# Kernel optimization log

Hardware: AMD Instinct MI355X
Metric: run time of the kernel (lower is better)

Reference implementation:

```python
import jax, jax.numpy as jnp
import numpy as np

EPS = 1e-5

def _ln(x, g, b):
    mu = x.mean(-1, keepdims=True)
    var = ((x - mu) ** 2).mean(-1, keepdims=True)
    return (x - mu) / jnp.sqrt(var + EPS) * g + b

def setup_inputs() -> dict:
    key = jax.random.key(0)
    ks = jax.random.split(key, 24)
    B, S, I, H, D, F = 64, 512, 32, 64, 128, 256
    def w(k, shape, fan_in):
        return jax.random.uniform(k, shape, jnp.float32, -1.0, 1.0) / np.sqrt(fan_in)
    return {
        'x': jax.random.normal(ks[0], (B, S, I), jnp.float32),
        'W_ih': w(ks[1], (H, I), H), 'b_ih': w(ks[2], (H,), H),
        'W_hh': w(ks[3], (H, H), H), 'b_hh': w(ks[4], (H,), H),
        'Wp': w(ks[5], (D, H), H), 'bp': w(ks[6], (D,), H),
        'Wqkv': w(ks[7], (3 * D, D), D), 'bqkv': jnp.zeros((3 * D,), jnp.float32),
        'Wo': w(ks[8], (D, D), D), 'bo': jnp.zeros((D,), jnp.float32),
        'g1': jnp.ones((D,), jnp.float32), 'be1': jnp.zeros((D,), jnp.float32),
        'W1': w(ks[9], (F, D), D), 'b1': w(ks[10], (F,), D),
        'W2': w(ks[11], (D, F), F), 'b2': w(ks[12], (D,), F),
        'g2': jnp.ones((D,), jnp.float32), 'be2': jnp.zeros((D,), jnp.float32),
        'gn': jnp.ones((D,), jnp.float32), 'bn': jnp.zeros((D,), jnp.float32),
        'Wf': w(ks[13], (I, D), D), 'bf': w(ks[14], (I,), D),
    }

def reference(x, W_ih, b_ih, W_hh, b_hh, Wp, bp, Wqkv, bqkv, Wo, bo,
              g1, be1, W1, b1, W2, b2, g2, be2, gn, bn, Wf, bf):
    B, S, I = x.shape
    H = W_ih.shape[0]
    D = Wp.shape[0]
    nh = 8
    hd = D // nh

    # RNNCell tanh recurrence over time (sequential, vectorized over batch)
    xs = jnp.swapaxes(x, 0, 1)  # (S, B, I)
    def step(h, x_t):
        h = jnp.tanh(x_t @ W_ih.T + b_ih + h @ W_hh.T + b_hh)
        return h, h
    _, hs = jax.lax.scan(step, jnp.zeros((B, H), x.dtype), xs)  # (S, B, H)

    proj = hs @ Wp.T + bp  # (S, B, D)

    # TransformerEncoderLayer (post-norm, relu), dropout = identity (eval)
    qkv = proj @ Wqkv.T + bqkv  # (S, B, 3D)
    q, k, v = jnp.split(qkv, 3, axis=-1)
    q = q.reshape(S, B, nh, hd)
    k = k.reshape(S, B, nh, hd)
    v = v.reshape(S, B, nh, hd)
    scores = jnp.einsum('sbhd,tbhd->bhst', q, k) / np.sqrt(hd)
    attn = jax.nn.softmax(scores, axis=-1)
    ctx = jnp.einsum('bhst,tbhd->sbhd', attn, v).reshape(S, B, D)
    attn_out = ctx @ Wo.T + bo
    x1 = _ln(proj + attn_out, g1, be1)
    ff = jax.nn.relu(x1 @ W1.T + b1) @ W2.T + b2
    x2 = _ln(x1 + ff, g2, be2)

    out = _ln(x2 + proj, gn, bn)
    pooled = out.mean(axis=0)  # (B, D)
    return jnp.tanh(pooled @ Wf.T + bf)
```

## Files before the change

### kernel.cpp

```cpp
#include <hip/hip_runtime.h>
#include <hip/hip_bf16.h>

#define BB 64
#define SS 512
#define II 32
#define HH 64
#define DD 128
#define FF 256
#define NHEAD 8
#define HDIM 16
#define NTOK (SS*BB)

typedef short bf16x8 __attribute__((ext_vector_type(8)));
typedef float f32x4  __attribute__((ext_vector_type(4)));

__device__ __forceinline__ float fast_tanh(float x) {
    float ax = fabsf(x);
    float e = __expf(-2.0f * ax);
    float r = (1.0f - e) * __builtin_amdgcn_rcpf(1.0f + e);
    return copysignf(r, x);
}

__device__ __forceinline__ float bcast(float v, int lane) {
    return __int_as_float(__builtin_amdgcn_readlane(__float_as_int(v), lane));
}

__device__ __forceinline__ short f2bf(float x) {
    unsigned u = __float_as_uint(x);
    return (short)((u + 0x7FFFu + ((u >> 16) & 1u)) >> 16);
}
__device__ __forceinline__ float bf2f(ushort u) {
    return __uint_as_float((unsigned)u << 16);
}

__global__ __launch_bounds__(256) void k_xw_wcvt(const float* __restrict__ x,
                                                 const float* __restrict__ W_ih,
                                                 const float* __restrict__ b_ih,
                                                 const float* __restrict__ b_hh,
                                                 float* __restrict__ xw,
                                                 const float* __restrict__ Wp,
                                                 const float* __restrict__ Wqkv,
                                                 const float* __restrict__ Wo,
                                                 const float* __restrict__ W1,
                                                 const float* __restrict__ W2,
                                                 ushort* __restrict__ wout) {
    if (blockIdx.x >= 8192) {
        int i = (blockIdx.x - 8192) * 256 + threadIdx.x;
        float v;
        if (i < 8192) v = Wp[i];
        else if (i < 57344) {
            int e = i - 8192;
            v = Wqkv[e];
            int row = e >> 7;
            if (row >= 128 && row < 256) v *= 0.36067376f;
        }
        else if (i < 73728) v = Wo[i - 57344];
        else if (i < 106496) v = W1[i - 73728];
        else v = W2[i - 106496];
        wout[i] = (ushort)f2bf(v);
        return;
    }
    int idx = blockIdx.x * 256 + threadIdx.x;
    int j  = idx & (HH - 1);
    int sb = idx >> 6;
    int s  = sb >> 6;
    int b  = sb & (BB - 1);
    const float* xr = x + (b * SS + s) * II;
    const float* wr = W_ih + j * II;
    float acc = b_ih[j] + b_hh[j];
    #pragma unroll
    for (int k = 0; k < II; k += 4) {
        float4 xv = *(const float4*)(xr + k);
        float4 wv = *(const float4*)(wr + k);
        acc += xv.x * wv.x + xv.y * wv.y + xv.z * wv.z + xv.w * wv.w;
    }
    xw[idx] = acc;
}

__global__ __launch_bounds__(64, 1) void k_rnn(const float* __restrict__ xw,
                                               const float* __restrict__ W_hh,
                                               float* __restrict__ hs) {
    int b = blockIdx.x;
    int j = threadIdx.x;
    float w[HH];
    #pragma unroll
    for (int k = 0; k < HH; k++) w[k] = W_hh[j * HH + k];

    float hv = 0.0f;
    float xv0 = xw[(0 * BB + b) * HH + j];
    float xv1 = xw[(1 * BB + b) * HH + j];
    for (int t = 0; t < SS; t++) {
        int tn = (t < SS - 2) ? t + 2 : t;
        float xnext = xw[(tn * BB + b) * HH + j];
        float a0 = xv0, a1 = 0.f, a2 = 0.f, a3 = 0.f;
        #pragma unroll
        for (int k = 0; k < HH; k += 4) {
            a0 = fmaf(w[k + 0], bcast(hv, k + 0), a0);
            a1 = fmaf(w[k + 1], bcast(hv, k + 1), a1);
            a2 = fmaf(w[k + 2], bcast(hv, k + 2), a2);
            a3 = fmaf(w[k + 3], bcast(hv, k + 3), a3);
        }
        hv = fast_tanh((a0 + a1) + (a2 + a3));
        hs[(t * BB + b) * HH + j] = hv;
        xv0 = xv1;
        xv1 = xnext;
    }
}

template<int K, bool RELU>
__global__ __launch_bounds__(256) void k_gemm_m64fa(const float* __restrict__ A,
                                                    const ushort* __restrict__ W,
                                                    const float* __restrict__ bias,
                                                    ushort* __restrict__ C, int N) {
    __shared__ short As[64 * 40];
    __shared__ short Ws[128 * 40];
    int tid = threadIdx.x;
    int wid = tid >> 6, lane = tid & 63;
    int col = lane & 15, quad = lane >> 4;
    int rowBase = blockIdx.x * 64, colBase = blockIdx.y * 128;

    f32x4 acc[8];
    #pragma unroll
    for (int nt = 0; nt < 8; nt++) {
        float bv = bias[colBase + nt * 16 + col];
        acc[nt][0] = bv; acc[nt][1] = bv; acc[nt][2] = bv; acc[nt][3] = bv;
    }

    int arow = tid >> 2, akc = (tid & 3) * 8;
    int wrow = tid >> 1, wkc = (tid & 1) * 16;

    for (int kb = 0; kb < K; kb += 32) {
        {
            const float4* ap = (const float4*)(A + (size_t)(rowBase + arow) * K + kb + akc);
            float4 v0 = ap[0], v1 = ap[1];
            short t0[8];
            t0[0]=f2bf(v0.x); t0[1]=f2bf(v0.y); t0[2]=f2bf(v0.z); t0[3]=f2bf(v0.w);
            t0[4]=f2bf(v1.x); t0[5]=f2bf(v1.y); t0[6]=f2bf(v1.z); t0[7]=f2bf(v1.w);
            *(int4*)&As[arow * 40 + akc] = *(int4*)t0;
        }
        {
            const int4* wp = (const int4*)(W + (size_t)(colBase + wrow) * K + kb + wkc);
            *(int4*)&Ws[wrow * 40 + wkc]     = wp[0];
            *(int4*)&Ws[wrow * 40 + wkc + 8] = wp[1];
        }
        __syncthreads();

        bf16x8 af = *(const bf16x8*)&As[(wid * 16 + col) * 40 + quad * 8];
        bf16x8 wf[8];
        #pragma unroll
        for (int nt = 0; nt < 8; nt++)
            wf[nt] = *(const bf16x8*)&Ws[(nt * 16 + col) * 40 + quad * 8];
        #pragma unroll
        for (int nt = 0; nt < 8; nt++)
            acc[nt] = __builtin_amdgcn_mfma_f32_16x16x32_bf16(af, wf[nt], acc[nt], 0, 0, 0);
        __syncthreads();
    }

    #pragma unroll
    for (int r = 0; r < 4; r++) {
        int m = rowBase + wid * 16 + quad * 4 + r;
        #pragma unroll
        for (int nt = 0; nt < 8; nt++) {
            float v = acc[nt][r];
            if (RELU) v = fmaxf(v, 0.f);
            C[(size_t)m * N + colBase + nt * 16 + col] = (ushort)f2bf(v);
        }
    }
}

template<int K, bool RELU, bool OUTBF>
__global__ __launch_bounds__(256) void k_gemm_m64b(const ushort* __restrict__ A,
                                                   const ushort* __restrict__ W,
                                                   const float* __restrict__ bias,
                                                   void* __restrict__ Cv, int N) {
    __shared__ short As[64 * 40];
    __shared__ short Ws[128 * 40];
    int tid = threadIdx.x;
    int wid = tid >> 6, lane = tid & 63;
    int col = lane & 15, quad = lane >> 4;
    int rowBase = blockIdx.x * 64, colBase = blockIdx.y * 128;

    f32x4 acc[8];
    #pragma unroll
    for (int nt = 0; nt < 8; nt++) {
        float bv = bias[colBase + nt * 16 + col];
        acc[nt][0] = bv; acc[nt][1] = bv; acc[nt][2] = bv; acc[nt][3] = bv;
    }

    int arow = tid >> 2, akc = (tid & 3) * 8;
    int wrow = tid >> 1, wkc = (tid & 1) * 16;

    for (int kb = 0; kb < K; kb += 32) {
        *(int4*)&As[arow * 40 + akc] =
            *(const int4*)(A + (size_t)(rowBase + arow) * K + kb + akc);
        {
            const int4* wp = (const int4*)(W + (size_t)(colBase + wrow) * K + kb + wkc);
            *(int4*)&Ws[wrow * 40 + wkc]     = wp[0];
            *(int4*)&Ws[wrow * 40 + wkc + 8] = wp[1];
        }
        __syncthreads();

        bf16x8 af = *(const bf16x8*)&As[(wid * 16 + col) * 40 + quad * 8];
        bf16x8 wf[8];
        #pragma unroll
        for (int nt = 0; nt < 8; nt++)
            wf[nt] = *(const bf16x8*)&Ws[(nt * 16 + col) * 40 + quad * 8];
        #pragma unroll
        for (int nt = 0; nt < 8; nt++)
            acc[nt] = __builtin_amdgcn_mfma_f32_16x16x32_bf16(af, wf[nt], acc[nt], 0, 0, 0);
        __syncthreads();
    }

    #pragma unroll
    for (int r = 0; r < 4; r++) {
        int m = rowBase + wid * 16 + quad * 4 + r;
        #pragma unroll
        for (int nt = 0; nt < 8; nt++) {
            float v = acc[nt][r];
            if (RELU) v = fmaxf(v, 0.f);
            if (OUTBF)
                ((ushort*)Cv)[(size_t)m * N + colBase + nt * 16 + col] = (ushort)f2bf(v);
            else
                ((float*)Cv)[(size_t)m * N + colBase + nt * 16 + col] = v;
        }
    }
}

template<int K, int NLN, bool OUTBF>
__global__ __launch_bounds__(256) void k_gemm_ln_m64b(const ushort* __restrict__ A,
                                                      const ushort* __restrict__ W,
                                                      const float* __restrict__ bias,
                                                      const ushort* __restrict__ res1,
                                                      const float* __restrict__ g1v,
                                                      const float* __restrict__ be1v,
                                                      const ushort* __restrict__ res2,
                                                      const float* __restrict__ g2v,
                                                      const float* __restrict__ be2v,
                                                      void* __restrict__ outv) {
    __shared__ short As[64 * 40];
    __shared__ short Ws[128 * 40];
    int tid = threadIdx.x;
    int wid = tid >> 6, lane = tid & 63;
    int col = lane & 15, quad = lane >> 4;
    int rowBase = blockIdx.x * 64;

    f32x4 acc[8];
    #pragma unroll
    for (int nt = 0; nt < 8; nt++) {
        float bv = bias[nt * 16 + col];
        acc[nt][0] = bv; acc[nt][1] = bv; acc[nt][2] = bv; acc[nt][3] = bv;
    }

    int arow = tid >> 2, akc = (tid & 3) * 8;
    int wrow = tid >> 1, wkc = (tid & 1) * 16;

    for (int kb = 0; kb < K; kb += 32) {
        *(int4*)&As[arow * 40 + akc] =
            *(const int4*)(A + (size_t)(rowBase + arow) * K + kb + akc);
        {
            const int4* wp = (const int4*)(W + (size_t)wrow * K + kb + wkc);
            *(int4*)&Ws[wrow * 40 + wkc]     = wp[0];
            *(int4*)&Ws[wrow * 40 + wkc + 8] = wp[1];
        }
        __syncthreads();

        bf16x8 af = *(const bf16x8*)&As[(wid * 16 + col) * 40 + quad * 8];
        bf16x8 wf[8];
        #pragma unroll
        for (int nt = 0; nt < 8; nt++)
            wf[nt] = *(const bf16x8*)&Ws[(nt * 16 + col) * 40 + quad * 8];
        #pragma unroll
        for (int nt = 0; nt < 8; nt++)
            acc[nt] = __builtin_amdgcn_mfma_f32_16x16x32_bf16(af, wf[nt], acc[nt], 0, 0, 0);
        __syncthreads();
    }

    float ga[8], ba[8], gb[8], bb[8];
    #pragma unroll
    for (int nt = 0; nt < 8; nt++) {
        ga[nt] = g1v[nt * 16 + col]; ba[nt] = be1v[nt * 16 + col];
        if (NLN == 2) { gb[nt] = g2v[nt * 16 + col]; bb[nt] = be2v[nt * 16 + col]; }
    }

    #pragma unroll
    for (int r = 0; r < 4; r++) {
        int m = rowBase + wid * 16 + quad * 4 + r;
        const ushort* rr1 = res1 + (size_t)m * DD;
        float v[8];
        float s = 0.f;
        #pragma unroll
        for (int nt = 0; nt < 8; nt++) {
            v[nt] = acc[nt][r] + bf2f(rr1[nt * 16 + col]);
            s += v[nt];
        }
        #pragma unroll
        for (int off = 1; off < 16; off <<= 1) s += __shfl_xor(s, off, 64);
        float mu = s * (1.0f / 128.0f);
        float vs = 0.f;
        #pragma unroll
        for (int nt = 0; nt < 8; nt++) { v[nt] -= mu; vs += v[nt] * v[nt]; }
        #pragma unroll
        for (int off = 1; off < 16; off <<= 1) vs += __shfl_xor(vs, off, 64);
        float rstd = rsqrtf(vs * (1.0f / 128.0f) + 1e-5f);
        #pragma unroll
        for (int nt = 0; nt < 8; nt++) v[nt] = v[nt] * rstd * ga[nt] + ba[nt];

        if (NLN == 2) {
            const ushort* rr2 = res2 + (size_t)m * DD;
            float s2 = 0.f;
            #pragma unroll
            for (int nt = 0; nt < 8; nt++) {
                v[nt] += bf2f(rr2[nt * 16 + col]);
                s2 += v[nt];
            }
            #pragma unroll
            for (int off = 1; off < 16; off <<= 1) s2 += __shfl_xor(s2, off, 64);
            float mu2 = s2 * (1.0f / 128.0f);
            float vs2 = 0.f;
            #pragma unroll
            for (int nt = 0; nt < 8; nt++) { v[nt] -= mu2; vs2 += v[nt] * v[nt]; }
            #pragma unroll
            for (int off = 1; off < 16; off <<= 1) vs2 += __shfl_xor(vs2, off, 64);
            float rstd2 = rsqrtf(vs2 * (1.0f / 128.0f) + 1e-5f);
            #pragma unroll
            for (int nt = 0; nt < 8; nt++) v[nt] = v[nt] * rstd2 * gb[nt] + bb[nt];
        }

        #pragma unroll
        for (int nt = 0; nt < 8; nt++) {
            if (OUTBF)
                ((ushort*)outv)[(size_t)m * DD + nt * 16 + col] = (ushort)f2bf(v[nt]);
            else
                ((float*)outv)[(size_t)m * DD + nt * 16 + col] = v[nt];
        }
    }
}

__global__ __launch_bounds__(256, 2) void k_attn(const ushort* __restrict__ qkv,
                                                 ushort* __restrict__ ctx) {
    int bh = blockIdx.x;
    int b = bh >> 3, h = bh & 7;
    __shared__ short Vt[HDIM][SS];
    __shared__ short Pb[4][2][16 * 64];
    int tid = threadIdx.x;

    for (int t = tid; t < SS; t += 256) {
        const ushort* base = qkv + (size_t)(t * BB + b) * 384 + 256 + h * 16;
        int4 va = *(const int4*)base;
        int4 vb = *(const int4*)(base + 8);
        const ushort* pa = (const ushort*)&va;
        const ushort* pb = (const ushort*)&vb;
        int u = t & 63;
        int pos = (t & ~63) | (((u & 15) << 2) | (u >> 4));
        #pragma unroll
        for (int d = 0; d < 8; d++) {
            Vt[d][pos]     = pa[d];
            Vt[d + 8][pos] = pb[d];
        }
    }
    __syncthreads();

    int wid = tid >> 6, lane = tid & 63;
    int col = lane & 15, quad = lane >> 4;

    bf16x8 kf[32];
    #pragma unroll
    for (int kt = 0; kt < 32; kt++) {
        bf16x8 f = (bf16x8)(short)0;
        if (quad < 2)
            f = *(const bf16x8*)(qkv + (size_t)((kt * 16 + col) * BB + b) * 384
                                 + 128 + h * 16 + quad * 8);
        kf[kt] = f;
    }

    for (int sub = 0; sub < 8; sub++) {
        int q0 = wid * 128 + sub * 16;

        bf16x8 qf = (bf16x8)(short)0;
        if (quad < 2)
            qf = *(const bf16x8*)(qkv + (size_t)((q0 + col) * BB + b) * 384
                                  + h * 16 + quad * 8);

        float l0 = 0.f, l1 = 0.f, l2 = 0.f, l3 = 0.f;
        f32x4 O = {0.f, 0.f, 0.f, 0.f};
        #pragma unroll
        for (int c = 0; c < 8; c++) {
            short* pbuf = &Pb[wid][c & 1][0];
            float p[4][4];
            #pragma unroll
            for (int kk = 0; kk < 4; kk++) {
                f32x4 z = {0.f, 0.f, 0.f, 0.f};
                f32x4 S = __builtin_amdgcn_mfma_f32_16x16x32_bf16(qf, kf[c * 4 + kk], z, 0, 0, 0);
                p[kk][0] = exp2f(S[0]); p[kk][1] = exp2f(S[1]);
                p[kk][2] = exp2f(S[2]); p[kk][3] = exp2f(S[3]);
                l0 += p[kk][0]; l1 += p[kk][1]; l2 += p[kk][2]; l3 += p[kk][3];
            }
            #pragma unroll
            for (int r = 0; r < 4; r++) {
                unsigned w0 = (unsigned)(unsigned short)f2bf(p[0][r])
                            | ((unsigned)(unsigned short)f2bf(p[1][r]) << 16);
                unsigned w1 = (unsigned)(unsigned short)f2bf(p[2][r])
                            | ((unsigned)(unsigned short)f2bf(p[3][r]) << 16);
                *(uint2*)&pbuf[(4 * quad + r) * 64 + col * 4] = make_uint2(w0, w1);
            }
            #pragma unroll
            for (int half = 0; half < 2; half++) {
                int tb = c * 64 + half * 32;
                bf16x8 pf = *(const bf16x8*)&pbuf[col * 64 + half * 32 + quad * 8];
                bf16x8 vf = *(const bf16x8*)&Vt[col][tb + quad * 8];
                O = __builtin_amdgcn_mfma_f32_16x16x32_bf16(pf, vf, O, 0, 0, 0);
            }
        }

        float l[4] = {l0, l1, l2, l3};
        #pragma unroll
        for (int r = 0; r < 4; r++) {
            #pragma unroll
            for (int off = 1; off < 16; off <<= 1) l[r] += __shfl_xor(l[r], off, 64);
            float inv = __builtin_amdgcn_rcpf(l[r]);
            int q = q0 + 4 * quad + r;
            ctx[(size_t)(q * BB + b) * DD + h * 16 + col] = (ushort)f2bf(O[r] * inv);
        }
    }
}

__global__ __launch_bounds__(256) void k_poolfinal(const float* __restrict__ outln,
                                                   const float* __restrict__ Wf,
                                                   const float* __restrict__ bfv,
                                                   float* __restrict__ out) {
    int b = blockIdx.x;
    int tid = threadIdx.x;
    __shared__ float part[256];
    __shared__ float pooled[128];
    int d = tid & 127, half = tid >> 7;
    float s = 0.f;
    int s0 = half * 256;
    #pragma unroll 8
    for (int si = s0; si < s0 + 256; si++)
        s += outln[(size_t)(si * BB + b) * DD + d];
    part[tid] = s;
    __syncthreads();
    if (tid < 128) pooled[tid] = (part[tid] + part[tid + 128]) * (1.0f / SS);
    __syncthreads();
    if (tid < 32) {
        const float* wr = Wf + tid * DD;
        float acc = bfv[tid];
        #pragma unroll
        for (int k = 0; k < DD; k += 4) {
            float4 wv = *(const float4*)(wr + k);
            acc += pooled[k] * wv.x + pooled[k + 1] * wv.y
                 + pooled[k + 2] * wv.z + pooled[k + 3] * wv.w;
        }
        out[b * 32 + tid] = fast_tanh(acc);
    }
}

extern "C" void kernel_launch(void* const* d_in, const int* in_sizes, int n_in,
                              void* d_out, int out_size, void* d_ws, size_t ws_size,
                              hipStream_t stream) {
    const float* x    = (const float*)d_in[0];
    const float* W_ih = (const float*)d_in[1];
    const float* b_ih = (const float*)d_in[2];
    const float* W_hh = (const float*)d_in[3];
    const float* b_hh = (const float*)d_in[4];
    const float* Wp   = (const float*)d_in[5];
    const float* bp   = (const float*)d_in[6];
    const float* Wqkv = (const float*)d_in[7];
    const float* bqkv = (const float*)d_in[8];
    const float* Wo   = (const float*)d_in[9];
    const float* bo   = (const float*)d_in[10];
    const float* g1   = (const float*)d_in[11];
    const float* be1  = (const float*)d_in[12];
    const float* W1   = (const float*)d_in[13];
    const float* b1   = (const float*)d_in[14];
    const float* W2   = (const float*)d_in[15];
    const float* b2   = (const float*)d_in[16];
    const float* g2   = (const float*)d_in[17];
    const float* be2  = (const float*)d_in[18];
    const float* gn   = (const float*)d_in[19];
    const float* bn   = (const float*)d_in[20];
    const float* Wf   = (const float*)d_in[21];
    const float* bf   = (const float*)d_in[22];
    float* out = (float*)d_out;
    char* wsb = (char*)d_ws;

    float*  xw    = (float*)(wsb);
    float*  hsf   = (float*)(wsb + (8u << 20));
    ushort* projb = (ushort*)(wsb + (16u << 20));
    ushort* qkvb  = (ushort*)(wsb + (24u << 20));
    ushort* ctxb  = (ushort*)(wsb + (48u << 20));
    ushort* x1b   = (ushort*)(wsb + (56u << 20));
    ushort* ff1b  = (ushort*)(wsb + (64u << 20));
    float*  outln = (float*)(wsb + (80u << 20));
    ushort* wbf   = (ushort*)(wsb + (96u << 20));
    ushort* Wp_bf   = wbf;
    ushort* Wqkv_bf = wbf + 8192;
    ushort* Wo_bf   = wbf + 57344;
    ushort* W1_bf   = wbf + 73728;
    ushort* W2_bf   = wbf + 106496;

    k_xw_wcvt<<<8736, 256, 0, stream>>>(x, W_ih, b_ih, b_hh, xw,
                                        Wp, Wqkv, Wo, W1, W2, wbf);
    k_rnn<<<64, 64, 0, stream>>>(xw, W_hh, hsf);
    k_gemm_m64fa<64, false><<<dim3(512, 1), 256, 0, stream>>>(hsf, Wp_bf, bp, projb, 128);
    k_gemm_m64b<128, false, true><<<dim3(512, 3), 256, 0, stream>>>(projb, Wqkv_bf, bqkv, qkvb, 384);
    k_attn<<<512, 256, 0, stream>>>(qkvb, ctxb);
    k_gemm_ln_m64b<128, 1, true><<<512, 256, 0, stream>>>(ctxb, Wo_bf, bo, projb, g1, be1,
                                                          nullptr, nullptr, nullptr, x1b);
    k_gemm_m64b<128, true, true><<<dim3(512, 2), 256, 0, stream>>>(x1b, W1_bf, b1, ff1b, 256);
    k_gemm_ln_m64b<256, 2, false><<<512, 256, 0, stream>>>(ff1b, W2_bf, b2, x1b, g2, be2,
                                                           projb, gn, bn, outln);
    k_poolfinal<<<64, 256, 0, stream>>>(outln, Wf, bf, out);
}
```

Measured before the change: 392.0 us.

## Overlap RNN recurrence with projection GEMMs via progress counters and flags

The RNN kernel now publishes a per-chunk progress counter after every 64 timesteps. The projection GEMM spin-waits on that counter before processing its rows, then sets a per-block completion flag, and the QKV GEMM spin-waits on that flag. The aim is to pipeline the sequential recurrence with the downstream GEMMs instead of running them strictly one after another. This only helps if same-stream kernels actually run concurrently. Otherwise it just adds a memset, atomics and polling overhead, and cross-kernel spin-waits carry residency and deadlock risk.

```diff
diff --git a/kernel.cpp b/kernel.cpp
--- a/kernel.cpp
+++ b/kernel.cpp
@@ -79,7 +79,8 @@
 
 __global__ __launch_bounds__(64, 1) void k_rnn(const float* __restrict__ xw,
                                                const float* __restrict__ W_hh,
-                                               float* __restrict__ hs) {
+                                               float* __restrict__ hs,
+                                               unsigned* __restrict__ prog) {
     int b = blockIdx.x;
     int j = threadIdx.x;
     float w[HH];
@@ -89,21 +90,27 @@
     float hv = 0.0f;
     float xv0 = xw[(0 * BB + b) * HH + j];
     float xv1 = xw[(1 * BB + b) * HH + j];
-    for (int t = 0; t < SS; t++) {
-        int tn = (t < SS - 2) ? t + 2 : t;
-        float xnext = xw[(tn * BB + b) * HH + j];
-        float a0 = xv0, a1 = 0.f, a2 = 0.f, a3 = 0.f;
-        #pragma unroll
-        for (int k = 0; k < HH; k += 4) {
-            a0 = fmaf(w[k + 0], bcast(hv, k + 0), a0);
-            a1 = fmaf(w[k + 1], bcast(hv, k + 1), a1);
-            a2 = fmaf(w[k + 2], bcast(hv, k + 2), a2);
-            a3 = fmaf(w[k + 3], bcast(hv, k + 3), a3);
-        }
-        hv = fast_tanh((a0 + a1) + (a2 + a3));
-        hs[(t * BB + b) * HH + j] = hv;
-        xv0 = xv1;
-        xv1 = xnext;
+    for (int tc = 0; tc < 8; tc++) {
+        for (int ti = 0; ti < 64; ti++) {
+            int t = tc * 64 + ti;
+            int tn = (t < SS - 2) ? t + 2 : t;
+            float xnext = xw[(tn * BB + b) * HH + j];
+            float a0 = xv0, a1 = 0.f, a2 = 0.f, a3 = 0.f;
+            #pragma unroll
+            for (int k = 0; k < HH; k += 4) {
+                a0 = fmaf(w[k + 0], bcast(hv, k + 0), a0);
+                a1 = fmaf(w[k + 1], bcast(hv, k + 1), a1);
+                a2 = fmaf(w[k + 2], bcast(hv, k + 2), a2);
+                a3 = fmaf(w[k + 3], bcast(hv, k + 3), a3);
+            }
+            hv = fast_tanh((a0 + a1) + (a2 + a3));
+            hs[(t * BB + b) * HH + j] = hv;
+            xv0 = xv1;
+            xv1 = xnext;
+        }
+        if (j == 0)
+            __hip_atomic_fetch_add(&prog[tc], 1u, __ATOMIC_RELEASE,
+                                   __HIP_MEMORY_SCOPE_AGENT);
     }
 }
 
@@ -111,7 +118,16 @@
 __global__ __launch_bounds__(256) void k_gemm_m64fa(const float* __restrict__ A,
                                                     const ushort* __restrict__ W,
                                                     const float* __restrict__ bias,
-                                                    ushort* __restrict__ C, int N) {
+                                                    ushort* __restrict__ C, int N,
+                                                    const unsigned* __restrict__ prog,
+                                                    unsigned* __restrict__ flags) {
+    if (threadIdx.x == 0) {
+        while (__hip_atomic_load(&prog[blockIdx.x >> 6], __ATOMIC_ACQUIRE,
+                                 __HIP_MEMORY_SCOPE_AGENT) < 64u)
+            __builtin_amdgcn_s_sleep(4);
+    }
+    __syncthreads();
+
     __shared__ short As[64 * 40];
     __shared__ short Ws[128 * 40];
     int tid = threadIdx.x;
@@ -166,13 +182,29 @@
             C[(size_t)m * N + colBase + nt * 16 + col] = (ushort)f2bf(v);
         }
     }
+
+    __threadfence();
+    __syncthreads();
+    if (threadIdx.x == 0)
+        __hip_atomic_store(&flags[blockIdx.x], 1u, __ATOMIC_RELEASE,
+                           __HIP_MEMORY_SCOPE_AGENT);
 }
 
 template<int K, bool RELU, bool OUTBF>
 __global__ __launch_bounds__(256) void k_gemm_m64b(const ushort* __restrict__ A,
                                                    const ushort* __restrict__ W,
                                                    const float* __restrict__ bias,
-                                                   void* __restrict__ Cv, int N) {
+                                                   void* __restrict__ Cv, int N,
+                                                   const unsigned* __restrict__ waitflag) {
+    if (waitflag) {
+        if (threadIdx.x == 0) {
+            while (__hip_atomic_load(&waitflag[blockIdx.x], __ATOMIC_ACQUIRE,
+                                     __HIP_MEMORY_SCOPE_AGENT) == 0u)
+                __builtin_amdgcn_s_sleep(4);
+        }
+        __syncthreads();
+    }
+
     __shared__ short As[64 * 40];
     __shared__ short Ws[128 * 40];
     int tid = threadIdx.x;
@@ -498,16 +530,23 @@
     ushort* Wo_bf   = wbf + 57344;
     ushort* W1_bf   = wbf + 73728;
     ushort* W2_bf   = wbf + 106496;
-
+    unsigned* sync  = (unsigned*)(wsb + (97u << 20));
+    unsigned* prog  = sync;
+    unsigned* flags = sync + 8;
+
+    hipMemsetAsync(sync, 0, (8 + 512) * sizeof(unsigned), stream);
     k_xw_wcvt<<<8736, 256, 0, stream>>>(x, W_ih, b_ih, b_hh, xw,
                                         Wp, Wqkv, Wo, W1, W2, wbf);
-    k_rnn<<<64, 64, 0, stream>>>(xw, W_hh, hsf);
-    k_gemm_m64fa<64, false><<<dim3(512, 1), 256, 0, stream>>>(hsf, Wp_bf, bp, projb, 128);
-    k_gemm_m64b<128, false, true><<<dim3(512, 3), 256, 0, stream>>>(projb, Wqkv_bf, bqkv, qkvb, 384);
+    k_rnn<<<64, 64, 0, stream>>>(xw, W_hh, hsf, prog);
+    k_gemm_m64fa<64, false><<<dim3(512, 1), 256, 0, stream>>>(hsf, Wp_bf, bp, projb, 128,
+                                                              prog, flags);
+    k_gemm_m64b<128, false, true><<<dim3(512, 3), 256, 0, stream>>>(projb, Wqkv_bf, bqkv,
+                                                                    qkvb, 384, flags);
     k_attn<<<512, 256, 0, stream>>>(qkvb, ctxb);
     k_gemm_ln_m64b<128, 1, true><<<512, 256, 0, stream>>>(ctxb, Wo_bf, bo, projb, g1, be1,
                                                           nullptr, nullptr, nullptr, x1b);
-    k_gemm_m64b<128, true, true><<<dim3(512, 2), 256, 0, stream>>>(x1b, W1_bf, b1, ff1b, 256);
+    k_gemm_m64b<128, true, true><<<dim3(512, 2), 256, 0, stream>>>(x1b, W1_bf, b1, ff1b,
+                                                                   256, nullptr);
     k_gemm_ln_m64b<256, 2, false><<<512, 256, 0, stream>>>(ff1b, W2_bf, b2, x1b, g2, be2,
                                                            projb, gn, bn, outln);
     k_poolfinal<<<64, 256, 0, stream>>>(outln, Wf, bf, out);
```

After: 493.0 us. 1.26x slower.

## Fold Wp into Wqkv and compute proj and qkv in one launch

Applied to the files above, without the earlier changes.

Precomputes a composed weight Wqkv·Wp (64-wide K) and bias in the prep kernel, so qkv is computed directly from the RNN hidden states instead of from the projected activations. The proj GEMM and the qkv GEMM now run as independent blocks of a single kernel, which removes one launch and the dependency on projb. This halves K for the qkv GEMM and lets both GEMMs run concurrently. The tradeoff is a naive per-thread 128-long dot product in the prep kernel and slightly different rounding, since qkv no longer passes through a bf16 proj intermediate.

```diff
diff --git a/kernel.cpp b/kernel.cpp
--- a/kernel.cpp
+++ b/kernel.cpp
@@ -43,17 +43,32 @@
                                                  const float* __restrict__ Wo,
                                                  const float* __restrict__ W1,
                                                  const float* __restrict__ W2,
-                                                 ushort* __restrict__ wout) {
+                                                 const float* __restrict__ bp,
+                                                 const float* __restrict__ bqkv,
+                                                 ushort* __restrict__ wout,
+                                                 ushort* __restrict__ Wq2,
+                                                 float* __restrict__ bq2) {
+    if (blockIdx.x >= 8736) {
+        int i = (blockIdx.x - 8736) * 256 + threadIdx.x;
+        int n = i >> 6, k = i & 63;
+        const float* wr = Wqkv + n * DD;
+        float acc = 0.f;
+        #pragma unroll 4
+        for (int d = 0; d < DD; d++) acc += wr[d] * Wp[d * HH + k];
+        float scale = (n >= 128 && n < 256) ? 0.36067376f : 1.0f;
+        Wq2[n * HH + k] = (ushort)f2bf(acc * scale);
+        if (k == 0) {
+            float bacc = bqkv[n];
+            for (int d = 0; d < DD; d++) bacc += wr[d] * bp[d];
+            bq2[n] = bacc * scale;
+        }
+        return;
+    }
     if (blockIdx.x >= 8192) {
         int i = (blockIdx.x - 8192) * 256 + threadIdx.x;
         float v;
         if (i < 8192) v = Wp[i];
-        else if (i < 57344) {
-            int e = i - 8192;
-            v = Wqkv[e];
-            int row = e >> 7;
-            if (row >= 128 && row < 256) v *= 0.36067376f;
-        }
+        else if (i < 57344) v = Wqkv[i - 8192];
         else if (i < 73728) v = Wo[i - 57344];
         else if (i < 106496) v = W1[i - 73728];
         else v = W2[i - 106496];
@@ -107,17 +122,30 @@
     }
 }
 
-template<int K, bool RELU>
-__global__ __launch_bounds__(256) void k_gemm_m64fa(const float* __restrict__ A,
-                                                    const ushort* __restrict__ W,
-                                                    const float* __restrict__ bias,
-                                                    ushort* __restrict__ C, int N) {
+__global__ __launch_bounds__(256) void k_projqkv(const float* __restrict__ hsf,
+                                                 const ushort* __restrict__ Wp_bf,
+                                                 const float* __restrict__ bp,
+                                                 ushort* __restrict__ projb,
+                                                 const ushort* __restrict__ Wq2,
+                                                 const float* __restrict__ bq2,
+                                                 ushort* __restrict__ qkvb) {
+    const int K = 64;
+    int bid = blockIdx.x;
+    const ushort* W; const float* bias; ushort* C; int N, rowBase, colBase;
+    if (bid < 512) {
+        W = Wp_bf; bias = bp; C = projb; N = 128;
+        rowBase = bid * 64; colBase = 0;
+    } else {
+        int e = bid - 512;
+        W = Wq2; bias = bq2; C = qkvb; N = 384;
+        rowBase = (e & 511) * 64; colBase = (e >> 9) * 128;
+    }
+
     __shared__ short As[64 * 40];
     __shared__ short Ws[128 * 40];
     int tid = threadIdx.x;
     int wid = tid >> 6, lane = tid & 63;
     int col = lane & 15, quad = lane >> 4;
-    int rowBase = blockIdx.x * 64, colBase = blockIdx.y * 128;
 
     f32x4 acc[8];
     #pragma unroll
@@ -129,9 +157,10 @@
     int arow = tid >> 2, akc = (tid & 3) * 8;
     int wrow = tid >> 1, wkc = (tid & 1) * 16;
 
+    #pragma unroll
     for (int kb = 0; kb < K; kb += 32) {
         {
-            const float4* ap = (const float4*)(A + (size_t)(rowBase + arow) * K + kb + akc);
+            const float4* ap = (const float4*)(hsf + (size_t)(rowBase + arow) * K + kb + akc);
             float4 v0 = ap[0], v1 = ap[1];
             short t0[8];
             t0[0]=f2bf(v0.x); t0[1]=f2bf(v0.y); t0[2]=f2bf(v0.z); t0[3]=f2bf(v0.w);
@@ -160,11 +189,8 @@
     for (int r = 0; r < 4; r++) {
         int m = rowBase + wid * 16 + quad * 4 + r;
         #pragma unroll
-        for (int nt = 0; nt < 8; nt++) {
-            float v = acc[nt][r];
-            if (RELU) v = fmaxf(v, 0.f);
-            C[(size_t)m * N + colBase + nt * 16 + col] = (ushort)f2bf(v);
-        }
+        for (int nt = 0; nt < 8; nt++)
+            C[(size_t)m * N + colBase + nt * 16 + col] = (ushort)f2bf(acc[nt][r]);
     }
 }
 
@@ -494,16 +520,17 @@
     float*  outln = (float*)(wsb + (80u << 20));
     ushort* wbf   = (ushort*)(wsb + (96u << 20));
     ushort* Wp_bf   = wbf;
-    ushort* Wqkv_bf = wbf + 8192;
     ushort* Wo_bf   = wbf + 57344;
     ushort* W1_bf   = wbf + 73728;
     ushort* W2_bf   = wbf + 106496;
-
-    k_xw_wcvt<<<8736, 256, 0, stream>>>(x, W_ih, b_ih, b_hh, xw,
-                                        Wp, Wqkv, Wo, W1, W2, wbf);
+    ushort* Wq2_bf  = wbf + 139264;
+    float*  bq2     = (float*)(wbf + 163840);
+
+    k_xw_wcvt<<<8832, 256, 0, stream>>>(x, W_ih, b_ih, b_hh, xw,
+                                        Wp, Wqkv, Wo, W1, W2, bp, bqkv,
+                                        wbf, Wq2_bf, bq2);
     k_rnn<<<64, 64, 0, stream>>>(xw, W_hh, hsf);
-    k_gemm_m64fa<64, false><<<dim3(512, 1), 256, 0, stream>>>(hsf, Wp_bf, bp, projb, 128);
-    k_gemm_m64b<128, false, true><<<dim3(512, 3), 256, 0, stream>>>(projb, Wqkv_bf, bqkv, qkvb, 384);
+    k_projqkv<<<2048, 256, 0, stream>>>(hsf, Wp_bf, bp, projb, Wq2_bf, bq2, qkvb);
     k_attn<<<512, 256, 0, stream>>>(qkvb, ctxb);
     k_gemm_ln_m64b<128, 1, true><<<512, 256, 0, stream>>>(ctxb, Wo_bf, bo, projb, g1, be1,
                                                           nullptr, nullptr, nullptr, x1b);
```

Measured after the change: 396.7 us. About the same (+1.2%).

## Fuse out-projection, LN1, FFN and final LayerNorms into one tail kernel

Applied to the files above, without the earlier changes.

Replaces three separate kernels (Wo GEMM plus LN1, W1 GEMM with ReLU, W2 GEMM plus two LNs) with a single per-64-row-tile kernel. The LN1 output and the FFN hidden activations stay in shared memory instead of round-tripping through global memory. W1 and W2 columns are permuted at conversion time to match the packed column order that the MFMA accumulator layout writes into LDS. This removes two launches and the global x1/ff1 traffic, at the cost of about 60KB of LDS per block, which lowers occupancy.

```diff
diff --git a/kernel.cpp b/kernel.cpp
--- a/kernel.cpp
+++ b/kernel.cpp
@@ -55,8 +55,15 @@
             if (row >= 128 && row < 256) v *= 0.36067376f;
         }
         else if (i < 73728) v = Wo[i - 57344];
-        else if (i < 106496) v = W1[i - 73728];
-        else v = W2[i - 106496];
+        else if (i < 106496) {
+            int e = i - 73728, n = e >> 7, p = e & 127;
+            v = W1[n * 128 + (p & 7) * 16 + (p >> 3)];
+        }
+        else {
+            int e = i - 106496, n = e >> 8, kp = e & 255;
+            int nc = kp >> 7, pl = kp & 127;
+            v = W2[n * 256 + nc * 128 + (pl & 7) * 16 + (pl >> 3)];
+        }
         wout[i] = (ushort)f2bf(v);
         return;
     }
@@ -226,73 +233,68 @@
     }
 }
 
-template<int K, int NLN, bool OUTBF>
-__global__ __launch_bounds__(256) void k_gemm_ln_m64b(const ushort* __restrict__ A,
-                                                      const ushort* __restrict__ W,
-                                                      const float* __restrict__ bias,
-                                                      const ushort* __restrict__ res1,
-                                                      const float* __restrict__ g1v,
-                                                      const float* __restrict__ be1v,
-                                                      const ushort* __restrict__ res2,
-                                                      const float* __restrict__ g2v,
-                                                      const float* __restrict__ be2v,
-                                                      void* __restrict__ outv) {
-    __shared__ short As[64 * 40];
-    __shared__ short Ws[128 * 40];
+__global__ __launch_bounds__(256) void k_tail(const ushort* __restrict__ ctx,
+                                              const ushort* __restrict__ Wo,
+                                              const float* __restrict__ bo,
+                                              const ushort* __restrict__ projb,
+                                              const float* __restrict__ g1v,
+                                              const float* __restrict__ be1v,
+                                              const ushort* __restrict__ W1p,
+                                              const float* __restrict__ b1v,
+                                              const ushort* __restrict__ W2p,
+                                              const float* __restrict__ b2v,
+                                              const float* __restrict__ g2v,
+                                              const float* __restrict__ be2v,
+                                              const float* __restrict__ gnv,
+                                              const float* __restrict__ bnv,
+                                              float* __restrict__ outln) {
+    __shared__ short smem[30720];
+    short* F1 = smem;
+    short* As = smem;
+    short* X1 = smem + 16896;
+    short* Ws = smem + 25600;
     int tid = threadIdx.x;
     int wid = tid >> 6, lane = tid & 63;
     int col = lane & 15, quad = lane >> 4;
     int rowBase = blockIdx.x * 64;
-
-    f32x4 acc[8];
-    #pragma unroll
-    for (int nt = 0; nt < 8; nt++) {
-        float bv = bias[nt * 16 + col];
-        acc[nt][0] = bv; acc[nt][1] = bv; acc[nt][2] = bv; acc[nt][3] = bv;
-    }
-
     int arow = tid >> 2, akc = (tid & 3) * 8;
     int wrow = tid >> 1, wkc = (tid & 1) * 16;
 
-    for (int kb = 0; kb < K; kb += 32) {
+    f32x4 acc[8];
+    #pragma unroll
+    for (int nt = 0; nt < 8; nt++) {
+        float bv = bo[nt * 16 + col];
+        acc[nt][0] = bv; acc[nt][1] = bv; acc[nt][2] = bv; acc[nt][3] = bv;
+    }
+    for (int kb = 0; kb < 128; kb += 32) {
         *(int4*)&As[arow * 40 + akc] =
-            *(const int4*)(A + (size_t)(rowBase + arow) * K + kb + akc);
+            *(const int4*)(ctx + (size_t)(rowBase + arow) * 128 + kb + akc);
         {
-            const int4* wp = (const int4*)(W + (size_t)wrow * K + kb + wkc);
+            const int4* wp = (const int4*)(Wo + (size_t)wrow * 128 + kb + wkc);
             *(int4*)&Ws[wrow * 40 + wkc]     = wp[0];
             *(int4*)&Ws[wrow * 40 + wkc + 8] = wp[1];
         }
         __syncthreads();
-
         bf16x8 af = *(const bf16x8*)&As[(wid * 16 + col) * 40 + quad * 8];
-        bf16x8 wf[8];
-        #pragma unroll
-        for (int nt = 0; nt < 8; nt++)
-            wf[nt] = *(const bf16x8*)&Ws[(nt * 16 + col) * 40 + quad * 8];
-        #pragma unroll
-        for (int nt = 0; nt < 8; nt++)
-            acc[nt] = __builtin_amdgcn_mfma_f32_16x16x32_bf16(af, wf[nt], acc[nt], 0, 0, 0);
-        __syncthreads();
-    }
-
-    float ga[8], ba[8], gb[8], bb[8];
-    #pragma unroll
-    for (int nt = 0; nt < 8; nt++) {
-        ga[nt] = g1v[nt * 16 + col]; ba[nt] = be1v[nt * 16 + col];
-        if (NLN == 2) { gb[nt] = g2v[nt * 16 + col]; bb[nt] = be2v[nt * 16 + col]; }
-    }
-
+        #pragma unroll
+        for (int nt = 0; nt < 8; nt++) {
+            bf16x8 wf = *(const bf16x8*)&Ws[(nt * 16 + col) * 40 + quad * 8];
+            acc[nt] = __builtin_amdgcn_mfma_f32_16x16x32_bf16(af, wf, acc[nt], 0, 0, 0);
+        }
+        __syncthreads();
+    }
+
+    float ga[8], ba[8];
+    #pragma unroll
+    for (int nt = 0; nt < 8; nt++) { ga[nt] = g1v[nt*16+col]; ba[nt] = be1v[nt*16+col]; }
     #pragma unroll
     for (int r = 0; r < 4; r++) {
-        int m = rowBase + wid * 16 + quad * 4 + r;
-        const ushort* rr1 = res1 + (size_t)m * DD;
+        int ml = wid * 16 + quad * 4 + r;
+        const ushort* rr1 = projb + (size_t)(rowBase + ml) * DD;
         float v[8];
         float s = 0.f;
         #pragma unroll
-        for (int nt = 0; nt < 8; nt++) {
-            v[nt] = acc[nt][r] + bf2f(rr1[nt * 16 + col]);
-            s += v[nt];
-        }
+        for (int nt = 0; nt < 8; nt++) { v[nt] = acc[nt][r] + bf2f(rr1[nt*16+col]); s += v[nt]; }
         #pragma unroll
         for (int off = 1; off < 16; off <<= 1) s += __shfl_xor(s, off, 64);
         float mu = s * (1.0f / 128.0f);
@@ -302,37 +304,111 @@
         #pragma unroll
         for (int off = 1; off < 16; off <<= 1) vs += __shfl_xor(vs, off, 64);
         float rstd = rsqrtf(vs * (1.0f / 128.0f) + 1e-5f);
-        #pragma unroll
-        for (int nt = 0; nt < 8; nt++) v[nt] = v[nt] * rstd * ga[nt] + ba[nt];
-
-        if (NLN == 2) {
-            const ushort* rr2 = res2 + (size_t)m * DD;
-            float s2 = 0.f;
+        short pk[8];
+        #pragma unroll
+        for (int nt = 0; nt < 8; nt++) pk[nt] = f2bf(v[nt] * rstd * ga[nt] + ba[nt]);
+        *(int4*)&X1[ml * 136 + col * 8] = *(int4*)pk;
+    }
+    __syncthreads();
+
+    #pragma unroll 1
+    for (int nc = 0; nc < 2; nc++) {
+        f32x4 acc2[8];
+        #pragma unroll
+        for (int nt = 0; nt < 8; nt++) {
+            float bv = b1v[nc * 128 + nt * 16 + col];
+            acc2[nt][0] = bv; acc2[nt][1] = bv; acc2[nt][2] = bv; acc2[nt][3] = bv;
+        }
+        for (int kb = 0; kb < 128; kb += 32) {
+            const int4* wp = (const int4*)(W1p + (size_t)(nc * 128 + wrow) * 128 + kb + wkc);
+            *(int4*)&Ws[wrow * 40 + wkc]     = wp[0];
+            *(int4*)&Ws[wrow * 40 + wkc + 8] = wp[1];
+            __syncthreads();
+            bf16x8 af = *(const bf16x8*)&X1[(wid * 16 + col) * 136 + kb + quad * 8];
             #pragma unroll
             for (int nt = 0; nt < 8; nt++) {
-                v[nt] += bf2f(rr2[nt * 16 + col]);
-                s2 += v[nt];
+                bf16x8 wf = *(const bf16x8*)&Ws[(nt * 16 + col) * 40 + quad * 8];
+                acc2[nt] = __builtin_amdgcn_mfma_f32_16x16x32_bf16(af, wf, acc2[nt], 0, 0, 0);
             }
+            __syncthreads();
+        }
+        #pragma unroll
+        for (int r = 0; r < 4; r++) {
+            int ml = wid * 16 + quad * 4 + r;
+            short pk[8];
             #pragma unroll
-            for (int off = 1; off < 16; off <<= 1) s2 += __shfl_xor(s2, off, 64);
-            float mu2 = s2 * (1.0f / 128.0f);
-            float vs2 = 0.f;
-            #pragma unroll
-            for (int nt = 0; nt < 8; nt++) { v[nt] -= mu2; vs2 += v[nt] * v[nt]; }
-            #pragma unroll
-            for (int off = 1; off < 16; off <<= 1) vs2 += __shfl_xor(vs2, off, 64);
-            float rstd2 = rsqrtf(vs2 * (1.0f / 128.0f) + 1e-5f);
-            #pragma unroll
-            for (int nt = 0; nt < 8; nt++) v[nt] = v[nt] * rstd2 * gb[nt] + bb[nt];
-        }
-
+            for (int nt = 0; nt < 8; nt++) pk[nt] = f2bf(fmaxf(acc2[nt][r], 0.f));
+            *(int4*)&F1[ml * 264 + nc * 128 + col * 8] = *(int4*)pk;
+        }
+    }
+    __syncthreads();
+
+    f32x4 acc3[8];
+    #pragma unroll
+    for (int nt = 0; nt < 8; nt++) {
+        float bv = b2v[nt * 16 + col];
+        acc3[nt][0] = bv; acc3[nt][1] = bv; acc3[nt][2] = bv; acc3[nt][3] = bv;
+    }
+    for (int kb = 0; kb < 256; kb += 32) {
+        const int4* wp = (const int4*)(W2p + (size_t)wrow * 256 + kb + wkc);
+        *(int4*)&Ws[wrow * 40 + wkc]     = wp[0];
+        *(int4*)&Ws[wrow * 40 + wkc + 8] = wp[1];
+        __syncthreads();
+        bf16x8 af = *(const bf16x8*)&F1[(wid * 16 + col) * 264 + kb + quad * 8];
         #pragma unroll
         for (int nt = 0; nt < 8; nt++) {
-            if (OUTBF)
-                ((ushort*)outv)[(size_t)m * DD + nt * 16 + col] = (ushort)f2bf(v[nt]);
-            else
-                ((float*)outv)[(size_t)m * DD + nt * 16 + col] = v[nt];
-        }
+            bf16x8 wf = *(const bf16x8*)&Ws[(nt * 16 + col) * 40 + quad * 8];
+            acc3[nt] = __builtin_amdgcn_mfma_f32_16x16x32_bf16(af, wf, acc3[nt], 0, 0, 0);
+        }
+        __syncthreads();
+    }
+
+    float g2a[8], b2a[8], gna[8], bna[8];
+    #pragma unroll
+    for (int nt = 0; nt < 8; nt++) {
+        g2a[nt] = g2v[nt*16+col]; b2a[nt] = be2v[nt*16+col];
+        gna[nt] = gnv[nt*16+col]; bna[nt] = bnv[nt*16+col];
+    }
+    #pragma unroll
+    for (int r = 0; r < 4; r++) {
+        int ml = wid * 16 + quad * 4 + r;
+        bf16x8 x1v = *(const bf16x8*)&X1[ml * 136 + col * 8];
+        float v[8];
+        float s = 0.f;
+        #pragma unroll
+        for (int nt = 0; nt < 8; nt++) {
+            v[nt] = acc3[nt][r] + bf2f((ushort)x1v[nt]);
+            s += v[nt];
+        }
+        #pragma unroll
+        for (int off = 1; off < 16; off <<= 1) s += __shfl_xor(s, off, 64);
+        float mu = s * (1.0f / 128.0f);
+        float vs = 0.f;
+        #pragma unroll
+        for (int nt = 0; nt < 8; nt++) { v[nt] -= mu; vs += v[nt] * v[nt]; }
+        #pragma unroll
+        for (int off = 1; off < 16; off <<= 1) vs += __shfl_xor(vs, off, 64);
+        float rstd = rsqrtf(vs * (1.0f / 128.0f) + 1e-5f);
+        #pragma unroll
+        for (int nt = 0; nt < 8; nt++) v[nt] = v[nt] * rstd * g2a[nt] + b2a[nt];
+
+        const ushort* rr2 = projb + (size_t)(rowBase + ml) * DD;
+        float s2 = 0.f;
+        #pragma unroll
+        for (int nt = 0; nt < 8; nt++) { v[nt] += bf2f(rr2[nt*16+col]); s2 += v[nt]; }
+        #pragma unroll
+        for (int off = 1; off < 16; off <<= 1) s2 += __shfl_xor(s2, off, 64);
+        float mu2 = s2 * (1.0f / 128.0f);
+        float vs2 = 0.f;
+        #pragma unroll
+        for (int nt = 0; nt < 8; nt++) { v[nt] -= mu2; vs2 += v[nt] * v[nt]; }
+        #pragma unroll
+        for (int off = 1; off < 16; off <<= 1) vs2 += __shfl_xor(vs2, off, 64);
+        float rstd2 = rsqrtf(vs2 * (1.0f / 128.0f) + 1e-5f);
+        float* orow = outln + (size_t)(rowBase + ml) * DD;
+        #pragma unroll
+        for (int nt = 0; nt < 8; nt++)
+            orow[nt * 16 + col] = v[nt] * rstd2 * gna[nt] + bna[nt];
     }
 }
 
@@ -489,26 +565,22 @@
     ushort* projb = (ushort*)(wsb + (16u << 20));
     ushort* qkvb  = (ushort*)(wsb + (24u << 20));
     ushort* ctxb  = (ushort*)(wsb + (48u << 20));
-    ushort* x1b   = (ushort*)(wsb + (56u << 20));
-    ushort* ff1b  = (ushort*)(wsb + (64u << 20));
-    float*  outln = (float*)(wsb + (80u << 20));
-    ushort* wbf   = (ushort*)(wsb + (96u << 20));
+    float*  outln = (float*)(wsb + (56u << 20));
+    ushort* wbf   = (ushort*)(wsb + (80u << 20));
     ushort* Wp_bf   = wbf;
     ushort* Wqkv_bf = wbf + 8192;
     ushort* Wo_bf   = wbf + 57344;
-    ushort* W1_bf   = wbf + 73728;
-    ushort* W2_bf   = wbf + 106496;
+    ushort* W1p_bf  = wbf + 73728;
+    ushort* W2p_bf  = wbf + 106496;
 
     k_xw_wcvt<<<8736, 256, 0, stream>>>(x, W_ih, b_ih, b_hh, xw,
                                         Wp, Wqkv, Wo, W1, W2, wbf);
     k_rnn<<<64, 64, 0, stream>>>(xw, W_hh, hsf);
     k_gemm_m64fa<64, false><<<dim3(512, 1), 256, 0, stream>>>(hsf, Wp_bf, bp, projb, 128);
-    k_gemm_m64b<128, false, true><<<dim3(512, 3), 256, 0, stream>>>(projb, Wqkv_bf, bqkv, qkvb, 384);
+    k_gemm_m64b<128, false, true><<<dim3(512, 3), 256, 0, stream>>>(projb, Wqkv_bf, bqkv,
+                                                                    qkvb, 384);
     k_attn<<<512, 256, 0, stream>>>(qkvb, ctxb);
-    k_gemm_ln_m64b<128, 1, true><<<512, 256, 0, stream>>>(ctxb, Wo_bf, bo, projb, g1, be1,
-                                                          nullptr, nullptr, nullptr, x1b);
-    k_gemm_m64b<128, true, true><<<dim3(512, 2), 256, 0, stream>>>(x1b, W1_bf, b1, ff1b, 256);
-    k_gemm_ln_m64b<256, 2, false><<<512, 256, 0, stream>>>(ff1b, W2_bf, b2, x1b, g2, be2,
-                                                           projb, gn, bn, outln);
+    k_tail<<<512, 256, 0, stream>>>(ctxb, Wo_bf, bo, projb, g1, be1,
+                                    W1p_bf, b1, W2p_bf, b2, g2, be2, gn, bn, outln);
     k_poolfinal<<<64, 256, 0, stream>>>(outln, Wf, bf, out);
 }
```

New measurement: 384.6 us. About the same (-1.9%).
